# Performance work log

Hardware: AMD Instinct MI355X
Metric: run time of the kernel (lower is better)

## Reference

```python
import jax, jax.numpy as jnp
import numpy as np

B, RULE_DIM, E, P, TOP_K = 8192, 128, 64, 16, 3
EPS = 1e-5
CONF_THRESH = 0.1


def _ln(x, g, b):
    # torch.nn.LayerNorm: biased variance, eps=1e-5
    m = x.mean(-1, keepdims=True)
    v = ((x - m) ** 2).mean(-1, keepdims=True)
    return (x - m) / jnp.sqrt(v + EPS) * g + b


def setup_inputs() -> dict:
    key = jax.random.key(0)
    ks = jax.random.split(key, 8)
    s = lambda fan: 1.0 / np.sqrt(fan)
    return {
        "rule_embedding": jax.random.normal(ks[0], (B, RULE_DIM), jnp.float32),
        "rp_w1": jax.random.normal(ks[1], (RULE_DIM, 256), jnp.float32) * s(RULE_DIM),
        "rp_b1": jnp.zeros((256,), jnp.float32),
        "rp_g1": jnp.ones((256,), jnp.float32),
        "rp_be1": jnp.zeros((256,), jnp.float32),
        "rp_w2": jax.random.normal(ks[2], (256, 512), jnp.float32) * s(256),
        "rp_b2": jnp.zeros((512,), jnp.float32),
        "rp_g2": jnp.ones((512,), jnp.float32),
        "rp_be2": jnp.zeros((512,), jnp.float32),
        "op_w": jax.random.normal(ks[3], (512, E), jnp.float32) * s(512),
        "op_b": jnp.zeros((E,), jnp.float32),
        "pe_w1": jax.random.normal(ks[4], (E, 512, 256), jnp.float32) * s(512),
        "pe_b1": jnp.zeros((E, 256), jnp.float32),
        "pe_g": jnp.ones((E, 256), jnp.float32),
        "pe_beta": jnp.zeros((E, 256), jnp.float32),
        "pe_w2": jax.random.normal(ks[5], (E, 256, P), jnp.float32) * s(256),
        "pe_b2": jnp.zeros((E, P), jnp.float32),
    }


def reference(rule_embedding, rp_w1, rp_b1, rp_g1, rp_be1, rp_w2, rp_b2,
              rp_g2, rp_be2, op_w, op_b, pe_w1, pe_b1, pe_g, pe_beta,
              pe_w2, pe_b2):
    # rule_parser: Linear -> LN -> ReLU -> Linear -> LN -> ReLU
    h = jax.nn.relu(_ln(rule_embedding @ rp_w1 + rp_b1, rp_g1, rp_be1))   # [B,256]
    features = jax.nn.relu(_ln(h @ rp_w2 + rp_b2, rp_g2, rp_be2))         # [B,512]

    # op routing: softmax + top-k
    op_probs = jax.nn.softmax(features @ op_w + op_b, axis=-1)            # [B,E]
    top_probs, top_idx = jax.lax.top_k(op_probs, TOP_K)                   # [B,K]

    # per-op param predictor MLP, evaluated for every expert (vmap over E)
    def expert(w1, b1, g, be, w2, b2):
        z = jax.nn.relu(_ln(features @ w1 + b1, g, be))                   # [B,256]
        return z @ w2 + b2                                                # [B,P]

    h2_all = jax.vmap(expert)(pe_w1, pe_b1, pe_g, pe_beta, pe_w2, pe_b2)  # [E,B,P]

    # gather the selected expert's raw param logits per (token, slot)
    params_sel = h2_all[top_idx, jnp.arange(B)[:, None], :]               # [B,K,P]

    # original skips ops with confidence < 0.1 -> mask them out
    mask = (top_probs >= CONF_THRESH).astype(params_sel.dtype)            # [B,K]
    params_out = params_sel * mask[..., None]

    return top_probs, top_idx, params_out
```

## Files before the change

kernel.cpp:

```cpp
#include <hip/hip_runtime.h>
#include <math.h>

#define Bv   8192
#define EPSv 1e-5f
#define CONFv 0.1f
#define MB (1024*1024)

typedef __attribute__((ext_vector_type(8))) short short8;
typedef __attribute__((ext_vector_type(4))) float f32x4;

__device__ __forceinline__ float wave_sum64(float v){
  #pragma unroll
  for (int o = 32; o; o >>= 1) v += __shfl_xor(v, o, 64);
  return v;
}

__device__ __forceinline__ void split3f(float x, short &h, short &m, short &l){
  unsigned u = __float_as_uint(x);
  h = (short)(u >> 16);
  float r1 = x - __uint_as_float(u & 0xffff0000u);
  unsigned u1 = __float_as_uint(r1);
  m = (short)(u1 >> 16);
  float r2 = r1 - __uint_as_float(u1 & 0xffff0000u);
  l = (short)(__float_as_uint(r2) >> 16);
}

__device__ __forceinline__ void split2f(float x, short &h, short &m){
  unsigned u = __float_as_uint(x);
  h = (short)(u >> 16);
  float r1 = x - __uint_as_float(u & 0xffff0000u);
  m = (short)(__float_as_uint(r1) >> 16);
}

__device__ __forceinline__ f32x4 mfma5(short8 ah, short8 am,
                                       short8 bh, short8 bm, short8 bl, f32x4 c){
  c = __builtin_amdgcn_mfma_f32_16x16x32_bf16(am, bm, c, 0, 0, 0);
  c = __builtin_amdgcn_mfma_f32_16x16x32_bf16(ah, bl, c, 0, 0, 0);
  c = __builtin_amdgcn_mfma_f32_16x16x32_bf16(am, bh, c, 0, 0, 0);
  c = __builtin_amdgcn_mfma_f32_16x16x32_bf16(ah, bm, c, 0, 0, 0);
  c = __builtin_amdgcn_mfma_f32_16x16x32_bf16(ah, bh, c, 0, 0, 0);
  return c;
}

__device__ __forceinline__ f32x4 mfma3(short8 ah, short8 al,
                                       short8 bh, short8 bl, f32x4 c){
  c = __builtin_amdgcn_mfma_f32_16x16x32_bf16(al, bh, c, 0, 0, 0);
  c = __builtin_amdgcn_mfma_f32_16x16x32_bf16(ah, bl, c, 0, 0, 0);
  c = __builtin_amdgcn_mfma_f32_16x16x32_bf16(ah, bh, c, 0, 0, 0);
  return c;
}

__global__ __launch_bounds__(256) void k_pack(const float* __restrict__ pw1,
    const float* __restrict__ pw2, const float* __restrict__ w1,
    const float* __restrict__ w2, const float* __restrict__ opw,
    unsigned short* __restrict__ p1, unsigned short* __restrict__ p2,
    unsigned short* __restrict__ w1p, unsigned short* __restrict__ w2p,
    unsigned short* __restrict__ opwp, int* __restrict__ cnt)
{
  int bid = blockIdx.x;
  if (bid < 4096){
    int t = bid*256 + threadIdx.x;
    int e = t >> 14, rem = t & 16383, kg = rem >> 8, n = rem & 255;
    const float* src = pw1 + ((size_t)e << 17) + (size_t)(kg*8)*256 + n;
    short8 h, l;
    #pragma unroll
    for (int j = 0; j < 8; j++){
      float w = src[(size_t)j*256];
      unsigned u = __float_as_uint(w);
      float r2 = w - __uint_as_float(u & 0xffff0000u);
      h[j] = (short)(u >> 16);
      l[j] = (short)(__float_as_uint(r2) >> 16);
    }
    int idx8 = ((((n >> 4)*16 + (kg >> 2))*64) + (kg & 3)*16 + (n & 15)) << 3;
    unsigned short* ep = p1 + (size_t)e * 262144;
    *(short8*)(ep + idx8)          = h;
    *(short8*)(ep + 131072 + idx8) = l;
  } else if (bid < 4224){
    int t = (bid - 4096)*256 + threadIdx.x;
    int e = t >> 9, rem = t & 511, kg = rem >> 4, n = rem & 15;
    const float* src = pw2 + (size_t)e*4096 + (size_t)(kg*8)*16 + n;
    short8 h, l;
    #pragma unroll
    for (int j = 0; j < 8; j++){
      float w = src[(size_t)j*16];
      unsigned u = __float_as_uint(w);
      float r2 = w - __uint_as_float(u & 0xffff0000u);
      h[j] = (short)(u >> 16);
      l[j] = (short)(__float_as_uint(r2) >> 16);
    }
    int idx8 = (((kg >> 2)*64) + (kg & 3)*16 + n) << 3;
    unsigned short* ep = p2 + (size_t)e * 8192;
    *(short8*)(ep + idx8)        = h;
    *(short8*)(ep + 4096 + idx8) = l;
  } else if (bid < 4352){
    int gid = (bid - 4224)*256 + threadIdx.x;
    int k = gid >> 8, n = gid & 255;
    short h, m, l;
    split3f(w1[gid], h, m, l);
    int idx = (((n >> 4)*4 + (k >> 5))*64 + (((k >> 3) & 3)*16 + (n & 15)))*8 + (k & 7);
    w1p[idx]             = (unsigned short)h;
    w1p[32768 + idx]     = (unsigned short)m;
    w1p[2*32768 + idx]   = (unsigned short)l;
  } else if (bid < 4864){
    int gid = (bid - 4352)*256 + threadIdx.x;
    int k = gid >> 9, n = gid & 511;
    short h, m, l;
    split3f(w2[gid], h, m, l);
    int idx = (((n >> 4)*8 + (k >> 5))*64 + (((k >> 3) & 3)*16 + (n & 15)))*8 + (k & 7);
    w2p[idx]             = (unsigned short)h;
    w2p[131072 + idx]    = (unsigned short)m;
    w2p[2*131072 + idx]  = (unsigned short)l;
  } else if (bid < 4992){
    int gid = (bid - 4864)*256 + threadIdx.x;
    int k = gid >> 6, n = gid & 63;
    short h, m, l;
    split3f(opw[gid], h, m, l);
    int idx = (((n >> 4)*16 + (k >> 5))*64 + (((k >> 3) & 3)*16 + (n & 15)))*8 + (k & 7);
    opwp[idx]            = (unsigned short)h;
    opwp[32768 + idx]    = (unsigned short)m;
    opwp[2*32768 + idx]  = (unsigned short)l;
  } else {
    if (threadIdx.x < 64) cnt[threadIdx.x] = 0;
  }
}

__global__ __launch_bounds__(1024) void k_fused(const float* __restrict__ X,
    const unsigned short* __restrict__ w1p, const float* __restrict__ b1,
    const float* __restrict__ g1, const float* __restrict__ be1,
    const unsigned short* __restrict__ w2p, const float* __restrict__ b2,
    const float* __restrict__ g2, const float* __restrict__ be2,
    const unsigned short* __restrict__ opwp, const float* __restrict__ opb,
    unsigned short* __restrict__ fh, unsigned short* __restrict__ fl,
    float* __restrict__ dout, int* __restrict__ cnt, int* __restrict__ list)
{
  extern __shared__ unsigned char smem[];
  unsigned short* xh  = (unsigned short*)smem;
  unsigned short* xm  = xh + 4096;
  unsigned short* hbh = xh + 8192;
  unsigned short* hbm = xh + 16384;
  unsigned short* gah = xh;
  unsigned short* gam = xh + 16384;
  __shared__ float ps[32][20];
  __shared__ float pq[32][20];
  __shared__ float mi[32][2];
  __shared__ float lg[32][64];

  const int tid = threadIdx.x;
  const int r0  = blockIdx.x * 32;
  const int wave = tid >> 6, lane = tid & 63, lquad = lane >> 4, l15 = lane & 15;

  {
    int r = tid >> 5, c4 = tid & 31;
    float4 v = ((const float4*)X)[(size_t)(r0+r)*32 + c4];
    unsigned u0 = __float_as_uint(v.x), u1 = __float_as_uint(v.y);
    unsigned u2 = __float_as_uint(v.z), u3 = __float_as_uint(v.w);
    float m0 = v.x - __uint_as_float(u0 & 0xffff0000u);
    float m1 = v.y - __uint_as_float(u1 & 0xffff0000u);
    float m2 = v.z - __uint_as_float(u2 & 0xffff0000u);
    float m3 = v.w - __uint_as_float(u3 & 0xffff0000u);
    unsigned hp0 = (u0 >> 16) | (u1 & 0xffff0000u);
    unsigned hp1 = (u2 >> 16) | (u3 & 0xffff0000u);
    unsigned mp0 = (__float_as_uint(m0) >> 16) | (__float_as_uint(m1) & 0xffff0000u);
    unsigned mp1 = (__float_as_uint(m2) >> 16) | (__float_as_uint(m3) & 0xffff0000u);
    int gk = c4 >> 1, half = c4 & 1;
    int off = r*128 + ((gk ^ (r & 7)) << 3) + half*4;
    ((unsigned*)(xh + off))[0] = hp0;
    ((unsigned*)(xh + off))[1] = hp1;
    ((unsigned*)(xm + off))[0] = mp0;
    ((unsigned*)(xm + off))[1] = mp1;
  }
  __syncthreads();

  float bcol1, gcol1, becol1;
  {
    int col = wave*16 + l15;
    bcol1 = b1[col]; gcol1 = g1[col]; becol1 = be1[col];
  }
  {
    f32x4 acc[2];
    acc[0] = (f32x4){0.f,0.f,0.f,0.f};
    acc[1] = (f32x4){0.f,0.f,0.f,0.f};
    const int pstride = 32768;
    for (int ks4 = 0; ks4 < 4; ks4++){
      const unsigned short* bp = w1p + (((wave*4 + ks4)*64 + lane) << 3);
      short8 bh = *(const short8*)bp;
      short8 bm = *(const short8*)(bp + pstride);
      short8 bl = *(const short8*)(bp + 2*pstride);
      #pragma unroll
      for (int mt = 0; mt < 2; mt++){
        int r = mt*16 + l15;
        int off = r*128 + (((ks4*4 + lquad) ^ (r & 7)) << 3);
        short8 ah = *(const short8*)(xh + off);
        short8 am = *(const short8*)(xm + off);
        acc[mt] = mfma5(ah, am, bh, bm, bl, acc[mt]);
      }
    }
    #pragma unroll
    for (int mt = 0; mt < 2; mt++)
      #pragma unroll
      for (int reg = 0; reg < 4; reg++){
        float z = acc[mt][reg] + bcol1;
        float s = z, q = z*z;
        #pragma unroll
        for (int o = 1; o < 16; o <<= 1){ s += __shfl_xor(s, o, 64); q += __shfl_xor(q, o, 64); }
        int row = mt*16 + lquad*4 + reg;
        if (l15 == 0){ ps[row][wave] = s; pq[row][wave] = q; }
      }
    __syncthreads();
    if (tid < 32){
      int row = tid;
      float4 s0 = *(const float4*)&ps[row][0],  s1 = *(const float4*)&ps[row][4];
      float4 s2 = *(const float4*)&ps[row][8],  s3 = *(const float4*)&ps[row][12];
      float4 q0 = *(const float4*)&pq[row][0],  q1 = *(const float4*)&pq[row][4];
      float4 q2 = *(const float4*)&pq[row][8],  q3 = *(const float4*)&pq[row][12];
      float s = s0.x; s += s0.y; s += s0.z; s += s0.w;
      s += s1.x; s += s1.y; s += s1.z; s += s1.w;
      s += s2.x; s += s2.y; s += s2.z; s += s2.w;
      s += s3.x; s += s3.y; s += s3.z; s += s3.w;
      float q = q0.x; q += q0.y; q += q0.z; q += q0.w;
      q += q1.x; q += q1.y; q += q1.z; q += q1.w;
      q += q2.x; q += q2.y; q += q2.z; q += q2.w;
      q += q3.x; q += q3.y; q += q3.z; q += q3.w;
      float mean = s * (1.0f/256.0f);
      float var  = q * (1.0f/256.0f) - mean*mean;
      mi[row][0] = mean;
      mi[row][1] = 1.0f / sqrtf(var + EPSv);
    }
    __syncthreads();
    #pragma unroll
    for (int mt = 0; mt < 2; mt++)
      #pragma unroll
      for (int reg = 0; reg < 4; reg++){
        int row = mt*16 + lquad*4 + reg;
        float2 mv = *(const float2*)mi[row];
        int col = wave*16 + l15;
        float z = acc[mt][reg] + bcol1;
        float y = fmaxf((z - mv.x)*mv.y*gcol1 + becol1, 0.f);
        short hh, mm2;
        split2f(y, hh, mm2);
        int gg = col >> 3, c7 = col & 7;
        int adr = row*256 + ((gg ^ (row & 7)) << 3) + c7;
        hbh[adr] = (unsigned short)hh;
        hbm[adr] = (unsigned short)mm2;
      }
  }
  __syncthreads();

  f32x4 acc2[2][2];
  #pragma unroll
  for (int mt = 0; mt < 2; mt++)
    #pragma unroll
    for (int nt = 0; nt < 2; nt++) acc2[mt][nt] = (f32x4){0.f,0.f,0.f,0.f};
  {
    const int pstride = 131072;
    for (int ks4 = 0; ks4 < 8; ks4++){
      short8 ah[2], am[2];
      #pragma unroll
      for (int mt = 0; mt < 2; mt++){
        int r = mt*16 + l15;
        int off = r*256 + (((ks4*4 + lquad) ^ (r & 7)) << 3);
        ah[mt] = *(const short8*)(hbh + off);
        am[mt] = *(const short8*)(hbm + off);
      }
      #pragma unroll
      for (int nt = 0; nt < 2; nt++){
        int ntg = wave*2 + nt;
        const unsigned short* bp = w2p + (((ntg*8 + ks4)*64 + lane) << 3);
        short8 bh = *(const short8*)bp;
        short8 bm = *(const short8*)(bp + pstride);
        short8 bl = *(const short8*)(bp + 2*pstride);
        #pragma unroll
        for (int mt = 0; mt < 2; mt++)
          acc2[mt][nt] = mfma5(ah[mt], am[mt], bh, bm, bl, acc2[mt][nt]);
      }
    }
  }

  float bcol[2], gcol[2], becol[2];
  #pragma unroll
  for (int nt = 0; nt < 2; nt++){
    int col = (wave*2 + nt)*16 + l15;
    bcol[nt] = b2[col]; gcol[nt] = g2[col]; becol[nt] = be2[col];
  }
  #pragma unroll
  for (int mt = 0; mt < 2; mt++)
    #pragma unroll
    for (int reg = 0; reg < 4; reg++){
      float s = 0.f, q = 0.f;
      #pragma unroll
      for (int nt = 0; nt < 2; nt++){
        float z = acc2[mt][nt][reg] + bcol[nt];
        s += z; q += z*z;
      }
      #pragma unroll
      for (int o = 1; o < 16; o <<= 1){ s += __shfl_xor(s, o, 64); q += __shfl_xor(q, o, 64); }
      int row = mt*16 + lquad*4 + reg;
      if (l15 == 0){ ps[row][wave] = s; pq[row][wave] = q; }
    }
  __syncthreads();
  if (tid < 32){
    int row = tid;
    float4 s0 = *(const float4*)&ps[row][0],  s1 = *(const float4*)&ps[row][4];
    float4 s2 = *(const float4*)&ps[row][8],  s3 = *(const float4*)&ps[row][12];
    float4 q0 = *(const float4*)&pq[row][0],  q1 = *(const float4*)&pq[row][4];
    float4 q2 = *(const float4*)&pq[row][8],  q3 = *(const float4*)&pq[row][12];
    float s = s0.x; s += s0.y; s += s0.z; s += s0.w;
    s += s1.x; s += s1.y; s += s1.z; s += s1.w;
    s += s2.x; s += s2.y; s += s2.z; s += s2.w;
    s += s3.x; s += s3.y; s += s3.z; s += s3.w;
    float q = q0.x; q += q0.y; q += q0.z; q += q0.w;
    q += q1.x; q += q1.y; q += q1.z; q += q1.w;
    q += q2.x; q += q2.y; q += q2.z; q += q2.w;
    q += q3.x; q += q3.y; q += q3.z; q += q3.w;
    float mean = s * (1.0f/512.0f);
    float var  = q * (1.0f/512.0f) - mean*mean;
    mi[row][0] = mean;
    mi[row][1] = 1.0f / sqrtf(var + EPSv);
  }
  __syncthreads();

  #pragma unroll
  for (int mt = 0; mt < 2; mt++)
    #pragma unroll
    for (int reg = 0; reg < 4; reg++){
      int row = mt*16 + lquad*4 + reg;
      float2 mv = *(const float2*)mi[row];
      #pragma unroll
      for (int nt = 0; nt < 2; nt++){
        int col = (wave*2 + nt)*16 + l15;
        float z = acc2[mt][nt][reg] + bcol[nt];
        float y = fmaxf((z - mv.x)*mv.y*gcol[nt] + becol[nt], 0.f);
        short hh, mm2;
        split2f(y, hh, mm2);
        int gg = col >> 3, c7 = col & 7;
        int adr = row*512 + ((gg ^ (row & 7)) << 3) + c7;
        gah[adr] = (unsigned short)hh;
        gam[adr] = (unsigned short)mm2;
      }
    }
  __syncthreads();

  if (wave < 4){
    f32x4 accg[2];
    accg[0] = (f32x4){0.f,0.f,0.f,0.f};
    accg[1] = (f32x4){0.f,0.f,0.f,0.f};
    for (int kt = 0; kt < 16; kt++){
      const unsigned short* bp = opwp + (((wave*16 + kt)*64 + lane) << 3);
      short8 bh = *(const short8*)bp;
      short8 bm = *(const short8*)(bp + 32768);
      short8 bl = *(const short8*)(bp + 65536);
      #pragma unroll
      for (int mt = 0; mt < 2; mt++){
        int r = mt*16 + l15;
        int off = r*512 + (((kt*4 + lquad) ^ (r & 7)) << 3);
        short8 ah = *(const short8*)(gah + off);
        short8 am = *(const short8*)(gam + off);
        accg[mt] = mfma5(ah, am, bh, bm, bl, accg[mt]);
      }
    }
    float opbv = opb[wave*16 + l15];
    #pragma unroll
    for (int mt = 0; mt < 2; mt++)
      #pragma unroll
      for (int reg = 0; reg < 4; reg++)
        lg[mt*16 + lquad*4 + reg][wave*16 + l15] = accg[mt][reg] + opbv;
  } else {
    int t4 = (wave - 4)*64 + lane;
    for (int i = t4; i < 4096; i += 768){
      int p = i >> 11, rem = i & 2047, r = rem >> 6, gg = rem & 63;
      short8 v = *(const short8*)((p ? gam : gah) + r*512 + ((gg ^ (r & 7)) << 3));
      unsigned short* dst = (p ? fl : fh) + (size_t)(r0 + r)*512 + gg*8;
      *(short8*)dst = v;
    }
  }
  __syncthreads();

  {
    for (int rr = 0; rr < 2; rr++){
      int r = wave*2 + rr, row = r0 + r;
      float l = lg[r][lane];
      float mx = l;
      #pragma unroll
      for (int o = 32; o; o >>= 1) mx = fmaxf(mx, __shfl_xor(mx, o, 64));
      float p = expf(l - mx);
      float s = wave_sum64(p);
      p /= s;
      float pv = p;
      for (int j = 0; j < 3; j++){
        float v = pv; int idx = lane;
        #pragma unroll
        for (int o = 32; o; o >>= 1){
          float ov = __shfl_xor(v, o, 64);
          int   oi = __shfl_xor(idx, o, 64);
          if (ov > v || (ov == v && oi < idx)){ v = ov; idx = oi; }
        }
        if (lane == 0){
          dout[(size_t)row*3 + j]                = v;
          dout[(size_t)Bv*3 + (size_t)row*3 + j] = (float)idx;
        }
        if (v >= CONFv){
          if (lane == 0){
            int pos = atomicAdd(&cnt[idx], 1);
            list[idx*Bv + pos] = (row << 2) | j;
          }
        } else {
          if (lane < 16) dout[(size_t)Bv*6 + (size_t)row*48 + j*16 + lane] = 0.f;
        }
        if (lane == idx) pv = -1.0f;
      }
    }
  }
}

__global__ __launch_bounds__(256) void k_expert(const unsigned short* __restrict__ fh,
    const unsigned short* __restrict__ fl,
    const unsigned short* __restrict__ p1, const float* __restrict__ b1,
    const float* __restrict__ g,  const float* __restrict__ beta,
    const unsigned short* __restrict__ p2, const float* __restrict__ b2,
    const int* __restrict__ cnt,  const int* __restrict__ list,
    float* __restrict__ dout)
{
  extern __shared__ unsigned char smem[];
  unsigned short* xh = (unsigned short*)smem;
  unsigned short* xl = xh + 32*512;
  float*          zs = (float*)smem;
  unsigned short* zp = (unsigned short*)smem;
  __shared__ int sdesc[3];

  const int tid = threadIdx.x;
  const int wave = tid >> 6, lane = tid & 63;
  const int lquad = lane >> 4, l15 = lane & 15;

  if (wave == 0){
    int c  = cnt[lane];
    int tl = (c + 31) >> 5;
    int incl = tl;
    #pragma unroll
    for (int o = 1; o < 64; o <<= 1){
      int v = __shfl_up(incl, o, 64);
      if (lane >= o) incl += v;
    }
    int total = __shfl(incl, 63, 64);
    int G   = (total + 7) >> 3;
    int grp = blockIdx.x & 7, rr = blockIdx.x >> 3;
    int lgc = grp*G + rr;
    int ok  = (G > 0) && (rr < G) && (lgc < total);
    unsigned long long bm = __ballot(ok && (incl > lgc));
    if (lane == 0){
      if (!ok || bm == 0ull){ sdesc[0] = -1; }
      else {
        int e = __ffsll((long long)bm) - 1;
        sdesc[0] = e; sdesc[1] = lgc; sdesc[2] = 0;
      }
    }
    if (bm != 0ull && ok){
      int e = __ffsll((long long)bm) - 1;
      int excl = __shfl(incl - tl, e, 64);
      int ne   = __shfl(c, e, 64);
      if (lane == 0){ sdesc[1] = lgc - excl; sdesc[2] = ne; }
    }
  }
  __syncthreads();
  const int e = sdesc[0];
  if (e < 0) return;
  const int t = sdesc[1];
  const int n = sdesc[2];
  const int base = t * 32;
  const int m = min(32, n - base);
  const int* lrow = list + e*Bv + base;

  for (int i = tid; i < 4096; i += 256){
    int p = i >> 11, rem = i & 2047, r = rem >> 6, gg = rem & 63;
    int ev = lrow[(r < m) ? r : 0];
    int row = ev >> 2;
    const unsigned short* src = (p ? fl : fh) + (size_t)row*512 + gg*8;
    short8 v = *(const short8*)src;
    unsigned short* dst = (p ? xl : xh) + r*512 + ((gg ^ (r & 7)) << 3);
    *(short8*)dst = v;
  }
  __syncthreads();

  const unsigned short* p1e = p1 + (size_t)e * 262144;
  const int colbase = wave * 64;
  f32x4 acc[2][4];
  #pragma unroll
  for (int mt = 0; mt < 2; mt++)
    #pragma unroll
    for (int nt = 0; nt < 4; nt++) acc[mt][nt] = (f32x4){0.f,0.f,0.f,0.f};

  for (int kt = 0; kt < 16; kt++){
    short8 ah[2], al[2];
    int gk = kt*4 + lquad;
    #pragma unroll
    for (int mt = 0; mt < 2; mt++){
      int r = mt*16 + l15;
      int off = r*512 + ((gk ^ (r & 7)) << 3);
      ah[mt] = *(const short8*)(xh + off);
      al[mt] = *(const short8*)(xl + off);
    }
    #pragma unroll
    for (int nt = 0; nt < 4; nt++){
      int ntg = wave*4 + nt;
      const unsigned short* bp = p1e + (((ntg*16 + kt)*64 + lane) << 3);
      short8 bh = *(const short8*)bp;
      short8 bl = *(const short8*)(bp + 131072);
      #pragma unroll
      for (int mt = 0; mt < 2; mt++)
        acc[mt][nt] = mfma3(ah[mt], al[mt], bh, bl, acc[mt][nt]);
    }
  }
  __syncthreads();

  #pragma unroll
  for (int nt = 0; nt < 4; nt++){
    int col = colbase + nt*16 + l15;
    float bb = b1[e*256 + col];
    #pragma unroll
    for (int mt = 0; mt < 2; mt++)
      #pragma unroll
      for (int rg = 0; rg < 4; rg++){
        int rl = mt*16 + lquad*4 + rg;
        zs[rl*264 + col] = acc[mt][nt][rg] + bb;
      }
  }
  __syncthreads();

  {
    float gv[4], bv[4];
    #pragma unroll
    for (int j = 0; j < 4; j++){
      gv[j] = g[e*256 + lane + 64*j];
      bv[j] = beta[e*256 + lane + 64*j];
    }
    for (int rr2 = 0; rr2 < 8; rr2++){
      int r = wave*8 + rr2;
      float x[4];
      float s = 0.f;
      #pragma unroll
      for (int j = 0; j < 4; j++){ x[j] = zs[r*264 + lane + 64*j]; s += x[j]; }
      s = wave_sum64(s);
      float mm = s * (1.0f/256.0f);
      float v = 0.f;
      #pragma unroll
      for (int j = 0; j < 4; j++){ float d = x[j] - mm; v += d*d; }
      v = wave_sum64(v) * (1.0f/256.0f);
      float inv = 1.0f / sqrtf(v + EPSv);
      #pragma unroll
      for (int j = 0; j < 4; j++){
        int c = lane + 64*j;
        float y = fmaxf((x[j] - mm)*inv*gv[j] + bv[j], 0.f);
        unsigned u = __float_as_uint(y);
        float res = y - __uint_as_float(u & 0xffff0000u);
        zp[r*528 + c]       = (unsigned short)(u >> 16);
        zp[r*528 + 264 + c] = (unsigned short)(__float_as_uint(res) >> 16);
      }
    }
  }
  __syncthreads();

  if (wave < 2){
    const unsigned short* p2e = p2 + (size_t)e * 8192;
    f32x4 acc2 = (f32x4){0.f,0.f,0.f,0.f};
    for (int kt2 = 0; kt2 < 8; kt2++){
      const unsigned short* zb = zp + (wave*16 + l15)*528 + kt2*32 + lquad*8;
      short8 ahh = *(const short8*)zb;
      short8 all2 = *(const short8*)(zb + 264);
      const unsigned short* bp = p2e + ((kt2*64 + lane) << 3);
      short8 bh = *(const short8*)bp;
      short8 bl = *(const short8*)(bp + 4096);
      acc2 = mfma3(ahh, all2, bh, bl, acc2);
    }
    float b2v = b2[e*16 + l15];
    #pragma unroll
    for (int reg = 0; reg < 4; reg++){
      int rl = wave*16 + lquad*4 + reg;
      if (rl < m){
        int ev = lrow[rl];
        int row = ev >> 2, j = ev & 3;
        dout[(size_t)Bv*6 + (size_t)row*48 + j*16 + l15] = acc2[reg] + b2v;
      }
    }
  }
}

extern "C" void kernel_launch(void* const* d_in, const int* in_sizes, int n_in,
                              void* d_out, int out_size, void* d_ws, size_t ws_size,
                              hipStream_t stream)
{
  const float* X   = (const float*)d_in[0];
  const float* w1  = (const float*)d_in[1];
  const float* b1  = (const float*)d_in[2];
  const float* g1  = (const float*)d_in[3];
  const float* be1 = (const float*)d_in[4];
  const float* w2  = (const float*)d_in[5];
  const float* b2  = (const float*)d_in[6];
  const float* g2  = (const float*)d_in[7];
  const float* be2 = (const float*)d_in[8];
  const float* opw = (const float*)d_in[9];
  const float* opb = (const float*)d_in[10];
  const float* pw1 = (const float*)d_in[11];
  const float* pb1 = (const float*)d_in[12];
  const float* pg  = (const float*)d_in[13];
  const float* pbe = (const float*)d_in[14];
  const float* pw2 = (const float*)d_in[15];
  const float* pb2 = (const float*)d_in[16];
  float* out = (float*)d_out;
  char*  ws  = (char*)d_ws;

  unsigned short* p1E    = (unsigned short*)ws;
  unsigned short* p2E    = (unsigned short*)(ws + (size_t)32*MB);
  unsigned short* w1p_rp = (unsigned short*)(ws + (size_t)33*MB);
  unsigned short* w2p_rp = (unsigned short*)(ws + (size_t)34*MB);
  unsigned short* opwp   = (unsigned short*)(ws + (size_t)35*MB);
  unsigned short* fh     = (unsigned short*)(ws + (size_t)36*MB);
  unsigned short* fl     = (unsigned short*)(ws + (size_t)44*MB);
  int*            list   = (int*)(ws + (size_t)52*MB);
  int*            cnt    = (int*)(ws + (size_t)54*MB);

  k_pack  <<<4993, 256, 0, stream>>>(pw1, pw2, w1, w2, opw, p1E, p2E,
                                     w1p_rp, w2p_rp, opwp, cnt);
  k_fused <<<256, 1024, 65536, stream>>>(X, w1p_rp, b1, g1, be1,
                                         w2p_rp, b2, g2, be2, opwp, opb,
                                         fh, fl, out, cnt, list);
  k_expert<<<832,  256, 65536, stream>>>(fh, fl, p1E, pb1, pg, pbe, p2E, pb2,
                                         cnt, list, out);
}
```

Measured before the change: 173.5 us.

## Fuse expert LayerNorm into MFMA registers and double k_expert waves

k_expert now launches 512 threads (8 waves), so each wave computes two 16-column tiles instead of four for the first expert GEMM. The LayerNorm epilogue no longer stages the fp32 pre-activations through shared memory. Each wave instead reduces per-row sum and sum-of-squares with lane shuffles, combines per-wave partials in a small LDS table, and then normalizes and splits the values straight from the accumulators. Variance is now computed as E[z^2]-mean^2, which is less numerically robust, and the extra waves add register and occupancy pressure.

```diff
diff --git a/kernel.cpp b/kernel.cpp
--- a/kernel.cpp
+++ b/kernel.cpp
@@ -412,7 +412,7 @@
   }
 }
 
-__global__ __launch_bounds__(256) void k_expert(const unsigned short* __restrict__ fh,
+__global__ __launch_bounds__(512) void k_expert(const unsigned short* __restrict__ fh,
     const unsigned short* __restrict__ fl,
     const unsigned short* __restrict__ p1, const float* __restrict__ b1,
     const float* __restrict__ g,  const float* __restrict__ beta,
@@ -423,8 +423,10 @@
   extern __shared__ unsigned char smem[];
   unsigned short* xh = (unsigned short*)smem;
   unsigned short* xl = xh + 32*512;
-  float*          zs = (float*)smem;
   unsigned short* zp = (unsigned short*)smem;
+  __shared__ float ps[32][12];
+  __shared__ float pq[32][12];
+  __shared__ float mi[32][2];
   __shared__ int sdesc[3];
 
   const int tid = threadIdx.x;
@@ -469,7 +471,7 @@
   const int m = min(32, n - base);
   const int* lrow = list + e*Bv + base;
 
-  for (int i = tid; i < 4096; i += 256){
+  for (int i = tid; i < 4096; i += 512){
     int p = i >> 11, rem = i & 2047, r = rem >> 6, gg = rem & 63;
     int ev = lrow[(r < m) ? r : 0];
     int row = ev >> 2;
@@ -481,12 +483,11 @@
   __syncthreads();
 
   const unsigned short* p1e = p1 + (size_t)e * 262144;
-  const int colbase = wave * 64;
-  f32x4 acc[2][4];
+  f32x4 acc[2][2];
   #pragma unroll
   for (int mt = 0; mt < 2; mt++)
     #pragma unroll
-    for (int nt = 0; nt < 4; nt++) acc[mt][nt] = (f32x4){0.f,0.f,0.f,0.f};
+    for (int nt = 0; nt < 2; nt++) acc[mt][nt] = (f32x4){0.f,0.f,0.f,0.f};
 
   for (int kt = 0; kt < 16; kt++){
     short8 ah[2], al[2];
@@ -499,8 +500,8 @@
       al[mt] = *(const short8*)(xl + off);
     }
     #pragma unroll
-    for (int nt = 0; nt < 4; nt++){
-      int ntg = wave*4 + nt;
+    for (int nt = 0; nt < 2; nt++){
+      int ntg = wave*2 + nt;
       const unsigned short* bp = p1e + (((ntg*16 + kt)*64 + lane) << 3);
       short8 bh = *(const short8*)bp;
       short8 bl = *(const short8*)(bp + 131072);
@@ -509,53 +510,63 @@
         acc[mt][nt] = mfma3(ah[mt], al[mt], bh, bl, acc[mt][nt]);
     }
   }
-  __syncthreads();
-
-  #pragma unroll
-  for (int nt = 0; nt < 4; nt++){
-    int col = colbase + nt*16 + l15;
-    float bb = b1[e*256 + col];
-    #pragma unroll
-    for (int mt = 0; mt < 2; mt++)
-      #pragma unroll
-      for (int rg = 0; rg < 4; rg++){
-        int rl = mt*16 + lquad*4 + rg;
-        zs[rl*264 + col] = acc[mt][nt][rg] + bb;
-      }
-  }
-  __syncthreads();
-
-  {
-    float gv[4], bv[4];
-    #pragma unroll
-    for (int j = 0; j < 4; j++){
-      gv[j] = g[e*256 + lane + 64*j];
-      bv[j] = beta[e*256 + lane + 64*j];
-    }
-    for (int rr2 = 0; rr2 < 8; rr2++){
-      int r = wave*8 + rr2;
-      float x[4];
-      float s = 0.f;
-      #pragma unroll
-      for (int j = 0; j < 4; j++){ x[j] = zs[r*264 + lane + 64*j]; s += x[j]; }
-      s = wave_sum64(s);
-      float mm = s * (1.0f/256.0f);
-      float v = 0.f;
-      #pragma unroll
-      for (int j = 0; j < 4; j++){ float d = x[j] - mm; v += d*d; }
-      v = wave_sum64(v) * (1.0f/256.0f);
-      float inv = 1.0f / sqrtf(v + EPSv);
-      #pragma unroll
-      for (int j = 0; j < 4; j++){
-        int c = lane + 64*j;
-        float y = fmaxf((x[j] - mm)*inv*gv[j] + bv[j], 0.f);
-        unsigned u = __float_as_uint(y);
-        float res = y - __uint_as_float(u & 0xffff0000u);
-        zp[r*528 + c]       = (unsigned short)(u >> 16);
-        zp[r*528 + 264 + c] = (unsigned short)(__float_as_uint(res) >> 16);
-      }
-    }
-  }
+
+  float bb[2], gv[2], bv[2];
+  #pragma unroll
+  for (int nt = 0; nt < 2; nt++){
+    int col = (wave*2 + nt)*16 + l15;
+    bb[nt] = b1[e*256 + col];
+    gv[nt] = g[e*256 + col];
+    bv[nt] = beta[e*256 + col];
+  }
+  #pragma unroll
+  for (int mt = 0; mt < 2; mt++)
+    #pragma unroll
+    for (int reg = 0; reg < 4; reg++){
+      float s = 0.f, q = 0.f;
+      #pragma unroll
+      for (int nt = 0; nt < 2; nt++){
+        float z = acc[mt][nt][reg] + bb[nt];
+        s += z; q += z*z;
+      }
+      #pragma unroll
+      for (int o = 1; o < 16; o <<= 1){ s += __shfl_xor(s, o, 64); q += __shfl_xor(q, o, 64); }
+      int row = mt*16 + lquad*4 + reg;
+      if (l15 == 0){ ps[row][wave] = s; pq[row][wave] = q; }
+    }
+  __syncthreads();
+  if (tid < 32){
+    int row = tid;
+    float4 s0 = *(const float4*)&ps[row][0], s1 = *(const float4*)&ps[row][4];
+    float4 q0 = *(const float4*)&pq[row][0], q1 = *(const float4*)&pq[row][4];
+    float s = s0.x; s += s0.y; s += s0.z; s += s0.w;
+    s += s1.x; s += s1.y; s += s1.z; s += s1.w;
+    float q = q0.x; q += q0.y; q += q0.z; q += q0.w;
+    q += q1.x; q += q1.y; q += q1.z; q += q1.w;
+    float mean = s * (1.0f/256.0f);
+    float var  = q * (1.0f/256.0f) - mean*mean;
+    mi[row][0] = mean;
+    mi[row][1] = 1.0f / sqrtf(var + EPSv);
+  }
+  __syncthreads();
+
+  #pragma unroll
+  for (int mt = 0; mt < 2; mt++)
+    #pragma unroll
+    for (int reg = 0; reg < 4; reg++){
+      int row = mt*16 + lquad*4 + reg;
+      float2 mv = *(const float2*)mi[row];
+      #pragma unroll
+      for (int nt = 0; nt < 2; nt++){
+        int col = (wave*2 + nt)*16 + l15;
+        float z = acc[mt][nt][reg] + bb[nt];
+        float y = fmaxf((z - mv.x)*mv.y*gv[nt] + bv[nt], 0.f);
+        short hh, mm2;
+        split2f(y, hh, mm2);
+        zp[row*528 + col]       = (unsigned short)hh;
+        zp[row*528 + 264 + col] = (unsigned short)mm2;
+      }
+    }
   __syncthreads();
 
   if (wave < 2){
@@ -622,6 +633,6 @@
   k_fused <<<256, 1024, 65536, stream>>>(X, w1p_rp, b1, g1, be1,
                                          w2p_rp, b2, g2, be2, opwp, opb,
                                          fh, fl, out, cnt, list);
-  k_expert<<<832,  256, 65536, stream>>>(fh, fl, p1E, pb1, pg, pbe, p2E, pb2,
+  k_expert<<<832,  512, 65536, stream>>>(fh, fl, p1E, pb1, pg, pbe, p2E, pb2,
                                          cnt, list, out);
 }
```

Measured after the change: 173.1 us. Within noise of the previous version (-0.2%).
